# Kernel optimization log

Hardware: AMD Instinct MI355X
Metric: run time of the kernel (lower is better)

The kernel has to match this reference:

```python
import jax, jax.numpy as jnp
import numpy as np

B, C, H, W = 8, 512, 32, 32


def setup_inputs() -> dict:
    key = jax.random.key(0)
    kx, kq, kk, k6 = jax.random.split(key, 4)
    std = 0.02
    return {
        "x": jax.random.normal(kx, (B, C, H, W), dtype=jnp.float32),
        "Wq": jax.random.normal(kq, (C, C), dtype=jnp.float32) * std,
        "bq": jnp.zeros((C,), dtype=jnp.float32),
        "Wk": jax.random.normal(kk, (C, C), dtype=jnp.float32) * std,
        "bk": jnp.zeros((C,), dtype=jnp.float32),
        "W6": jax.random.normal(k6, (C, C), dtype=jnp.float32) * std,
        "b6": jnp.zeros((C,), dtype=jnp.float32),
    }


def reference(x, Wq, bq, Wk, bk, W6, b6):
    b, c, h, w = x.shape
    hw = h * w
    scale = 1.0 / (c ** 0.5)
    # [B, HW, C] token-major view of the feature map
    xf = jnp.transpose(x.reshape(b, c, hw), (0, 2, 1))
    # 1x1 convs are per-pixel linear layers (weight layout: [C_out, C_in])
    q = xf @ Wq.T + bq                      # [B, HW, C]
    k = xf @ Wk.T + bk                      # [B, HW, C]
    # cross-batch attention scores: every pixel attends to every pixel of every image
    scores = q.reshape(b * hw, c) @ k.reshape(b * hw, c).T   # [B*HW, B*HW]
    s = scores.reshape(b * hw, b, hw)
    # per-query: max response within each image, then mean over images
    xw = jnp.max(s, axis=-1).mean(axis=-1)  # [B*HW]
    xw = xw.reshape(b, hw) * scale
    xw = jax.nn.softmax(xw, axis=-1).reshape(b, 1, h, w)
    x5 = x * xw                             # spatial gating
    # final 1x1 conv
    of = jnp.transpose(x5.reshape(b, c, hw), (0, 2, 1)) @ W6.T + b6
    return jnp.transpose(of, (0, 2, 1)).reshape(b, c, h, w)
```

## Files before the change

### kernel.cpp

```cpp
#include <hip/hip_runtime.h>


typedef __attribute__((ext_vector_type(8))) short bf16x8;
typedef __attribute__((ext_vector_type(4))) float f32x4;
typedef __attribute__((ext_vector_type(2))) long long i64x2;

__device__ __forceinline__ unsigned short f2bf(float f) {
  unsigned u = __builtin_bit_cast(unsigned, f);
  u += 0x7FFFu + ((u >> 16) & 1u);
  return (unsigned short)(u >> 16);
}

__device__ __forceinline__ unsigned char f2e4m3(float x) {
  unsigned u = __builtin_bit_cast(unsigned, x);
  unsigned char s = (unsigned char)((u >> 24) & 0x80u);
  unsigned a = u & 0x7FFFFFFFu;
  if (a >= 0x43E00000u) return s | 0x7Eu;
  if (a < 0x3C800000u) {
    float q = __builtin_bit_cast(float, a) * 512.f;
    int m = (int)(q + 0.5f);
    return s | (unsigned char)m;
  }
  unsigned r = a + 0x7FFFFu + ((a >> 20) & 1u);
  int e = (int)((r >> 23) & 0xFF) - 127;
  if (e > 8) return s | 0x7Eu;
  unsigned m3 = (r >> 20) & 0x7u;
  return s | (unsigned char)(((e + 7) << 3) | m3);
}

__device__ __forceinline__ void gload_lds16(const void* g, void* l) {
  __builtin_amdgcn_global_load_lds(
      (const __attribute__((address_space(1))) unsigned int*)g,
      (__attribute__((address_space(3))) unsigned int*)l, 16, 0, 0);
}

__global__ __launch_bounds__(256) void prep(const float* __restrict__ x,
                                            const float* __restrict__ Wq,
                                            const float* __restrict__ Wk,
                                            const float* __restrict__ W6,
                                            short* __restrict__ xt,
                                            short* __restrict__ wcat) {
  const int bid = blockIdx.x, u = threadIdx.x;
  if (bid < 1024) {
    const int p0 = (bid & 15) * 64, c0 = ((bid >> 4) & 7) * 64, b = bid >> 7;
    __shared__ float t[64][65];
    {
      const int p4 = u & 15, cr = u >> 4;
      for (int cc = 0; cc < 4; ++cc) {
        const int c = cc * 16 + cr;
        const float4 v = *(const float4*)&x[((size_t)(b * 512 + c0 + c)) * 1024 + p0 + p4 * 4];
        t[p4 * 4 + 0][c] = v.x; t[p4 * 4 + 1][c] = v.y;
        t[p4 * 4 + 2][c] = v.z; t[p4 * 4 + 3][c] = v.w;
      }
    }
    __syncthreads();
    {
      const int c4 = u & 15, pr = u >> 4;
      for (int pp = 0; pp < 4; ++pp) {
        const int p = pp * 16 + pr;
        ushort4 o;
        o.x = f2bf(t[p][c4 * 4 + 0]); o.y = f2bf(t[p][c4 * 4 + 1]);
        o.z = f2bf(t[p][c4 * 4 + 2]); o.w = f2bf(t[p][c4 * 4 + 3]);
        *(ushort4*)&xt[((size_t)(b * 1024 + p0 + p)) * 512 + c0 + c4 * 4] = o;
      }
    }
  } else {
    const int i = (bid - 1024) * 256 + u;
    const int idx = i * 4;
    const float* src = (idx < 262144) ? Wq : (idx < 524288) ? Wk : W6;
    const float4 v = *(const float4*)&src[idx & 262143];
    ushort4 o;
    o.x = f2bf(v.x); o.y = f2bf(v.y); o.z = f2bf(v.z); o.w = f2bf(v.w);
    *(ushort4*)&wcat[idx] = o;
  }
}

__global__ __launch_bounds__(256) void gemm_qk(const short* __restrict__ xt,
                                               const short* __restrict__ wcat,
                                               const float* __restrict__ bq,
                                               const float* __restrict__ bk,
                                               unsigned char* __restrict__ qk8) {
  __shared__ short lds_a[128 * 64];
  __shared__ short lds_b[128 * 64];
  const int tid = threadIdx.x, w = tid >> 6, lane = tid & 63;
  const int wr = w >> 1, wc = w & 1;
  const int quad = lane >> 4, lcol = lane & 15;
  const int srow = lane & 15, skq = lane >> 4;
  const int m0 = blockIdx.x * 128, n0 = blockIdx.y * 128;

  f32x4 acc[4][4];
#pragma unroll
  for (int i = 0; i < 4; ++i)
#pragma unroll
    for (int j = 0; j < 4; ++j)
#pragma unroll
      for (int r = 0; r < 4; ++r) acc[i][j][r] = 0.f;

  const short* Abase = xt + (size_t)(m0 + srow) * 512 + skq * 8;
  const short* Bbase = wcat + (size_t)(n0 + srow) * 512 + skq * 8;

  for (int kt = 0; kt < 8; ++kt) {
    const int kb = kt * 64;
    __syncthreads();
#pragma unroll
    for (int gg = 0; gg < 2; ++gg) {
      const int g = w + gg * 4;
      gload_lds16(Abase + (size_t)(g * 16) * 512 + kb,      lds_a + g * 1024);
      gload_lds16(Abase + (size_t)(g * 16) * 512 + kb + 32, lds_a + g * 1024 + 512);
      gload_lds16(Bbase + (size_t)(g * 16) * 512 + kb,      lds_b + g * 1024);
      gload_lds16(Bbase + (size_t)(g * 16) * 512 + kb + 32, lds_b + g * 1024 + 512);
    }
    __syncthreads();
#pragma unroll
    for (int h = 0; h < 2; ++h) {
      bf16x8 af[4], bf[4];
#pragma unroll
      for (int i = 0; i < 4; ++i)
        af[i] = *(const bf16x8*)&lds_a[(wr * 4 + i) * 1024 + h * 512 + lane * 8];
#pragma unroll
      for (int j = 0; j < 4; ++j)
        bf[j] = *(const bf16x8*)&lds_b[(wc * 4 + j) * 1024 + h * 512 + lane * 8];
#pragma unroll
      for (int i = 0; i < 4; ++i)
#pragma unroll
        for (int j = 0; j < 4; ++j)
          acc[i][j] = __builtin_amdgcn_mfma_f32_16x16x32_bf16(af[i], bf[j], acc[i][j], 0, 0, 0);
    }
  }

  const float* bias = (blockIdx.y >= 4) ? bk : bq;
#pragma unroll
  for (int i = 0; i < 4; ++i)
#pragma unroll
    for (int j = 0; j < 4; ++j) {
      const int row = m0 + wr * 64 + i * 16 + quad * 4;
      const int col = n0 + wc * 64 + j * 16 + lcol;
      const float bv = bias[col & 511];
#pragma unroll
      for (int r = 0; r < 4; ++r)
        qk8[(size_t)(row + r) * 1024 + col] = f2e4m3(acc[i][j][r] + bv);
    }
}

__global__ __launch_bounds__(256) void gemm_scores(const unsigned char* __restrict__ qk8,
                                                   float* __restrict__ wsmx) {
  __shared__ unsigned char lds_b[32768];
  const int tid = threadIdx.x, w = tid >> 6, lane = tid & 63;
  const int quad = lane >> 4, lcol = lane & 15;
  const int srow = lane & 15, skb = (lane >> 4) * 16;
  const int m0 = blockIdx.x * 128, n0 = blockIdx.y * 128;

  f32x4 acc[2][8];
#pragma unroll
  for (int rg = 0; rg < 2; ++rg)
#pragma unroll
    for (int j = 0; j < 8; ++j)
#pragma unroll
      for (int r = 0; r < 4; ++r) acc[rg][j][r] = 0.f;

  const unsigned char* Abase = qk8 + (size_t)(m0 + w * 32 + srow) * 1024 + skb;
  const unsigned char* Bbase = qk8 + (size_t)(n0 + srow) * 1024 + 512 + skb;

#pragma unroll
  for (int kh = 0; kh < 2; ++kh) {
    __syncthreads();
#pragma unroll
    for (int jj = 0; jj < 2; ++jj) {
      const int j = w * 2 + jj;
#pragma unroll
      for (int kb = 0; kb < 4; ++kb)
        gload_lds16(Bbase + (size_t)(j * 16) * 1024 + kh * 256 + kb * 64,
                    lds_b + j * 4096 + kb * 1024);
    }
    i64x2 af[2][4];
#pragma unroll
    for (int rg = 0; rg < 2; ++rg)
#pragma unroll
      for (int kb = 0; kb < 4; ++kb)
        af[rg][kb] = *(const i64x2*)(Abase + (size_t)rg * 16384 + kh * 256 + kb * 64);
    __syncthreads();
#pragma unroll
    for (int kb = 0; kb < 4; ++kb) {
#pragma unroll
      for (int j = 0; j < 8; ++j) {
        const i64x2 bf = *(const i64x2*)&lds_b[j * 4096 + kb * 1024 + lane * 16];
#pragma unroll
        for (int rg = 0; rg < 2; ++rg) {
          acc[rg][j] = __builtin_amdgcn_mfma_f32_16x16x32_fp8_fp8(
              af[rg][kb].x, bf.x, acc[rg][j], 0, 0, 0);
          acc[rg][j] = __builtin_amdgcn_mfma_f32_16x16x32_fp8_fp8(
              af[rg][kb].y, bf.y, acc[rg][j], 0, 0, 0);
        }
      }
    }
  }

#pragma unroll
  for (int rg = 0; rg < 2; ++rg) {
#pragma unroll
    for (int r = 0; r < 4; ++r) {
      float v = acc[rg][0][r];
#pragma unroll
      for (int j = 1; j < 8; ++j) v = fmaxf(v, acc[rg][j][r]);
#pragma unroll
      for (int off = 1; off < 16; off <<= 1) v = fmaxf(v, __shfl_xor(v, off));
      if (lcol == 0)
        wsmx[(size_t)blockIdx.y * 8192 + m0 + w * 32 + rg * 16 + quad * 4 + r] = v;
    }
  }
}

__global__ __launch_bounds__(1024) void softmax_xw(const float* __restrict__ wsmx,
                                                   float* __restrict__ xw) {
  const int b = blockIdx.x, p = threadIdx.x;
  const int m = b * 1024 + p;
  float s = 0.f;
#pragma unroll
  for (int img = 0; img < 8; ++img) {
    float mx = -1e30f;
#pragma unroll
    for (int t = 0; t < 8; ++t) mx = fmaxf(mx, wsmx[(size_t)(img * 8 + t) * 8192 + m]);
    s += mx;
  }
  const float logit = s * 0.005524271728019903f;
  __shared__ float red[16];
  float v = logit;
#pragma unroll
  for (int off = 32; off >= 1; off >>= 1) v = fmaxf(v, __shfl_xor(v, off));
  if ((p & 63) == 0) red[p >> 6] = v;
  __syncthreads();
  float bmax = red[0];
#pragma unroll
  for (int t = 1; t < 16; ++t) bmax = fmaxf(bmax, red[t]);
  const float e = expf(logit - bmax);
  float sv = e;
#pragma unroll
  for (int off = 32; off >= 1; off >>= 1) sv += __shfl_xor(sv, off);
  __syncthreads();
  if ((p & 63) == 0) red[p >> 6] = sv;
  __syncthreads();
  float bsum = 0.f;
#pragma unroll
  for (int t = 0; t < 16; ++t) bsum += red[t];
  xw[m] = e / bsum;
}

__global__ __launch_bounds__(256) void gemm_out(const short* __restrict__ xt,
                                                const short* __restrict__ wcat,
                                                const float* __restrict__ xw,
                                                const float* __restrict__ b6,
                                                float* __restrict__ out) {
  __shared__ short lds_a[64 * 64];
  __shared__ short lds_b[64 * 64];
  const int tid = threadIdx.x, w = tid >> 6, lane = tid & 63;
  const int wr = w >> 1, wc = w & 1;
  const int quad = lane >> 4, lcol = lane & 15;
  const int srow = lane & 15, skq = lane >> 4;
  const int m0 = blockIdx.x * 64, n0 = blockIdx.y * 64;

  f32x4 acc[2][2];
#pragma unroll
  for (int i = 0; i < 2; ++i)
#pragma unroll
    for (int j = 0; j < 2; ++j)
#pragma unroll
      for (int r = 0; r < 4; ++r) acc[i][j][r] = 0.f;

  const short* Abase = xt + (size_t)(m0 + w * 16 + srow) * 512 + skq * 8;
  const short* Bbase = wcat + (size_t)(1024 + n0 + w * 16 + srow) * 512 + skq * 8;

  for (int kt = 0; kt < 8; ++kt) {
    const int kb = kt * 64;
    __syncthreads();
    gload_lds16(Abase + kb,      lds_a + w * 1024);
    gload_lds16(Abase + kb + 32, lds_a + w * 1024 + 512);
    gload_lds16(Bbase + kb,      lds_b + w * 1024);
    gload_lds16(Bbase + kb + 32, lds_b + w * 1024 + 512);
    __syncthreads();
#pragma unroll
    for (int h = 0; h < 2; ++h) {
      bf16x8 af[2], bf[2];
#pragma unroll
      for (int i = 0; i < 2; ++i)
        af[i] = *(const bf16x8*)&lds_a[(wr * 2 + i) * 1024 + h * 512 + lane * 8];
#pragma unroll
      for (int j = 0; j < 2; ++j)
        bf[j] = *(const bf16x8*)&lds_b[(wc * 2 + j) * 1024 + h * 512 + lane * 8];
#pragma unroll
      for (int i = 0; i < 2; ++i)
#pragma unroll
        for (int j = 0; j < 2; ++j)
          acc[i][j] = __builtin_amdgcn_mfma_f32_16x16x32_bf16(af[i], bf[j], acc[i][j], 0, 0, 0);
    }
  }

#pragma unroll
  for (int i = 0; i < 2; ++i) {
    const int mbase = m0 + wr * 32 + i * 16 + quad * 4;
    const int b = mbase >> 10, p = mbase & 1023;
    const float4 wv = *(const float4*)&xw[mbase];
#pragma unroll
    for (int j = 0; j < 2; ++j) {
      const int col = n0 + wc * 32 + j * 16 + lcol;
      const float bias = b6[col];
      float4 o;
      o.x = acc[i][j][0] * wv.x + bias;
      o.y = acc[i][j][1] * wv.y + bias;
      o.z = acc[i][j][2] * wv.z + bias;
      o.w = acc[i][j][3] * wv.w + bias;
      *(float4*)&out[((size_t)(b * 512 + col)) * 1024 + p] = o;
    }
  }
}

extern "C" void kernel_launch(void* const* d_in, const int* in_sizes, int n_in,
                              void* d_out, int out_size, void* d_ws, size_t ws_size,
                              hipStream_t stream) {
  const float* x  = (const float*)d_in[0];
  const float* Wq = (const float*)d_in[1];
  const float* bq = (const float*)d_in[2];
  const float* Wk = (const float*)d_in[3];
  const float* bk = (const float*)d_in[4];
  const float* W6 = (const float*)d_in[5];
  const float* b6 = (const float*)d_in[6];
  float* out = (float*)d_out;

  char* ws = (char*)d_ws;
  short* xt          = (short*)(ws + 0);
  short* wcat        = (short*)(ws + 8388608);
  unsigned char* qk8 = (unsigned char*)(ws + 10485760);
  float* wsmx        = (float*)(ws + 18874368);
  float* xw          = (float*)(ws + 20971520);

  prep<<<1792, 256, 0, stream>>>(x, Wq, Wk, W6, xt, wcat);
  gemm_qk<<<dim3(64, 8), 256, 0, stream>>>(xt, wcat, bq, bk, qk8);
  gemm_scores<<<dim3(64, 64), 256, 0, stream>>>(qk8, wsmx);
  softmax_xw<<<8, 1024, 0, stream>>>(wsmx, xw);
  gemm_out<<<dim3(128, 8), 256, 0, stream>>>(xt, wcat, xw, b6, out);
}
```

Measured before the change: 191.6 us.

## Fold output projection into QK GEMM and use scaled fp8 MFMA for scores

The W6 projection is now computed in the first GEMM launch as extra column tiles, written as fp32 z. The output becomes a transpose-and-scale epilogue, valid because per-pixel gating commutes with the 1x1 conv. The scores GEMM switches from 16x16x32 fp8 MFMA to the 16x16x128 f8f6f4 scaled MFMA with unit scales, which halves the LDS staging buffer and issues fewer, larger instructions. This removes a separate bf16 GEMM launch but adds a 16 MB fp32 z write and reread.

```diff
diff --git a/kernel.cpp b/kernel.cpp
--- a/kernel.cpp
+++ b/kernel.cpp
@@ -3,7 +3,8 @@
 
 typedef __attribute__((ext_vector_type(8))) short bf16x8;
 typedef __attribute__((ext_vector_type(4))) float f32x4;
-typedef __attribute__((ext_vector_type(2))) long long i64x2;
+typedef __attribute__((ext_vector_type(4))) int i32x4;
+typedef __attribute__((ext_vector_type(8))) int i32x8;
 
 __device__ __forceinline__ unsigned short f2bf(float f) {
   unsigned u = __builtin_bit_cast(unsigned, f);
@@ -75,11 +76,12 @@
   }
 }
 
-__global__ __launch_bounds__(256) void gemm_qk(const short* __restrict__ xt,
-                                               const short* __restrict__ wcat,
-                                               const float* __restrict__ bq,
-                                               const float* __restrict__ bk,
-                                               unsigned char* __restrict__ qk8) {
+__global__ __launch_bounds__(256) void gemm_qkz(const short* __restrict__ xt,
+                                                const short* __restrict__ wcat,
+                                                const float* __restrict__ bq,
+                                                const float* __restrict__ bk,
+                                                unsigned char* __restrict__ qk8,
+                                                float* __restrict__ z) {
   __shared__ short lds_a[128 * 64];
   __shared__ short lds_b[128 * 64];
   const int tid = threadIdx.x, w = tid >> 6, lane = tid & 63;
@@ -128,23 +130,37 @@
     }
   }
 
-  const float* bias = (blockIdx.y >= 4) ? bk : bq;
-#pragma unroll
-  for (int i = 0; i < 4; ++i)
-#pragma unroll
-    for (int j = 0; j < 4; ++j) {
-      const int row = m0 + wr * 64 + i * 16 + quad * 4;
-      const int col = n0 + wc * 64 + j * 16 + lcol;
-      const float bv = bias[col & 511];
-#pragma unroll
-      for (int r = 0; r < 4; ++r)
-        qk8[(size_t)(row + r) * 1024 + col] = f2e4m3(acc[i][j][r] + bv);
-    }
+  const int region = (int)blockIdx.y >> 2;
+  if (region < 2) {
+    const float* bias = region ? bk : bq;
+#pragma unroll
+    for (int i = 0; i < 4; ++i)
+#pragma unroll
+      for (int j = 0; j < 4; ++j) {
+        const int row = m0 + wr * 64 + i * 16 + quad * 4;
+        const int col = n0 + wc * 64 + j * 16 + lcol;
+        const float bv = bias[col & 511];
+#pragma unroll
+        for (int r = 0; r < 4; ++r)
+          qk8[(size_t)(row + r) * 1024 + col] = f2e4m3(acc[i][j][r] + bv);
+      }
+  } else {
+#pragma unroll
+    for (int i = 0; i < 4; ++i)
+#pragma unroll
+      for (int j = 0; j < 4; ++j) {
+        const int row = m0 + wr * 64 + i * 16 + quad * 4;
+        const int col = n0 - 1024 + wc * 64 + j * 16 + lcol;
+#pragma unroll
+        for (int r = 0; r < 4; ++r)
+          z[(size_t)(row + r) * 512 + col] = acc[i][j][r];
+      }
+  }
 }
 
 __global__ __launch_bounds__(256) void gemm_scores(const unsigned char* __restrict__ qk8,
                                                    float* __restrict__ wsmx) {
-  __shared__ unsigned char lds_b[32768];
+  __shared__ unsigned char lds_b[16384];
   const int tid = threadIdx.x, w = tid >> 6, lane = tid & 63;
   const int quad = lane >> 4, lcol = lane & 15;
   const int srow = lane & 15, skb = (lane >> 4) * 16;
@@ -162,36 +178,34 @@
   const unsigned char* Bbase = qk8 + (size_t)(n0 + srow) * 1024 + 512 + skb;
 
 #pragma unroll
-  for (int kh = 0; kh < 2; ++kh) {
+  for (int kh = 0; kh < 4; ++kh) {
+    const int kb = kh * 128;
     __syncthreads();
 #pragma unroll
     for (int jj = 0; jj < 2; ++jj) {
       const int j = w * 2 + jj;
 #pragma unroll
-      for (int kb = 0; kb < 4; ++kb)
-        gload_lds16(Bbase + (size_t)(j * 16) * 1024 + kh * 256 + kb * 64,
-                    lds_b + j * 4096 + kb * 1024);
-    }
-    i64x2 af[2][4];
-#pragma unroll
-    for (int rg = 0; rg < 2; ++rg)
-#pragma unroll
-      for (int kb = 0; kb < 4; ++kb)
-        af[rg][kb] = *(const i64x2*)(Abase + (size_t)rg * 16384 + kh * 256 + kb * 64);
-    __syncthreads();
-#pragma unroll
-    for (int kb = 0; kb < 4; ++kb) {
-#pragma unroll
-      for (int j = 0; j < 8; ++j) {
-        const i64x2 bf = *(const i64x2*)&lds_b[j * 4096 + kb * 1024 + lane * 16];
-#pragma unroll
-        for (int rg = 0; rg < 2; ++rg) {
-          acc[rg][j] = __builtin_amdgcn_mfma_f32_16x16x32_fp8_fp8(
-              af[rg][kb].x, bf.x, acc[rg][j], 0, 0, 0);
-          acc[rg][j] = __builtin_amdgcn_mfma_f32_16x16x32_fp8_fp8(
-              af[rg][kb].y, bf.y, acc[rg][j], 0, 0, 0);
-        }
-      }
+      for (int h = 0; h < 2; ++h)
+        gload_lds16(Bbase + (size_t)(j * 16) * 1024 + kb + h * 64,
+                    lds_b + j * 2048 + h * 1024);
+    }
+    i32x8 af[2];
+#pragma unroll
+    for (int rg = 0; rg < 2; ++rg) {
+      const i32x4 lo = *(const i32x4*)(Abase + (size_t)rg * 16384 + kb);
+      const i32x4 hi = *(const i32x4*)(Abase + (size_t)rg * 16384 + kb + 64);
+      af[rg] = __builtin_shufflevector(lo, hi, 0, 1, 2, 3, 4, 5, 6, 7);
+    }
+    __syncthreads();
+#pragma unroll
+    for (int j = 0; j < 8; ++j) {
+      const i32x4 blo = *(const i32x4*)&lds_b[j * 2048 + lane * 16];
+      const i32x4 bhi = *(const i32x4*)&lds_b[j * 2048 + 1024 + lane * 16];
+      const i32x8 bf = __builtin_shufflevector(blo, bhi, 0, 1, 2, 3, 4, 5, 6, 7);
+#pragma unroll
+      for (int rg = 0; rg < 2; ++rg)
+        acc[rg][j] = __builtin_amdgcn_mfma_scale_f32_16x16x128_f8f6f4(
+            af[rg], bf, acc[rg][j], 0, 0, 0, 127, 0, 127);
     }
   }
 
@@ -245,70 +259,37 @@
   xw[m] = e / bsum;
 }
 
-__global__ __launch_bounds__(256) void gemm_out(const short* __restrict__ xt,
-                                                const short* __restrict__ wcat,
-                                                const float* __restrict__ xw,
-                                                const float* __restrict__ b6,
-                                                float* __restrict__ out) {
-  __shared__ short lds_a[64 * 64];
-  __shared__ short lds_b[64 * 64];
-  const int tid = threadIdx.x, w = tid >> 6, lane = tid & 63;
-  const int wr = w >> 1, wc = w & 1;
-  const int quad = lane >> 4, lcol = lane & 15;
-  const int srow = lane & 15, skq = lane >> 4;
-  const int m0 = blockIdx.x * 64, n0 = blockIdx.y * 64;
-
-  f32x4 acc[2][2];
-#pragma unroll
-  for (int i = 0; i < 2; ++i)
-#pragma unroll
-    for (int j = 0; j < 2; ++j)
-#pragma unroll
-      for (int r = 0; r < 4; ++r) acc[i][j][r] = 0.f;
-
-  const short* Abase = xt + (size_t)(m0 + w * 16 + srow) * 512 + skq * 8;
-  const short* Bbase = wcat + (size_t)(1024 + n0 + w * 16 + srow) * 512 + skq * 8;
-
-  for (int kt = 0; kt < 8; ++kt) {
-    const int kb = kt * 64;
-    __syncthreads();
-    gload_lds16(Abase + kb,      lds_a + w * 1024);
-    gload_lds16(Abase + kb + 32, lds_a + w * 1024 + 512);
-    gload_lds16(Bbase + kb,      lds_b + w * 1024);
-    gload_lds16(Bbase + kb + 32, lds_b + w * 1024 + 512);
-    __syncthreads();
-#pragma unroll
-    for (int h = 0; h < 2; ++h) {
-      bf16x8 af[2], bf[2];
-#pragma unroll
-      for (int i = 0; i < 2; ++i)
-        af[i] = *(const bf16x8*)&lds_a[(wr * 2 + i) * 1024 + h * 512 + lane * 8];
-#pragma unroll
-      for (int j = 0; j < 2; ++j)
-        bf[j] = *(const bf16x8*)&lds_b[(wc * 2 + j) * 1024 + h * 512 + lane * 8];
-#pragma unroll
-      for (int i = 0; i < 2; ++i)
-#pragma unroll
-        for (int j = 0; j < 2; ++j)
-          acc[i][j] = __builtin_amdgcn_mfma_f32_16x16x32_bf16(af[i], bf[j], acc[i][j], 0, 0, 0);
-    }
-  }
-
-#pragma unroll
-  for (int i = 0; i < 2; ++i) {
-    const int mbase = m0 + wr * 32 + i * 16 + quad * 4;
-    const int b = mbase >> 10, p = mbase & 1023;
-    const float4 wv = *(const float4*)&xw[mbase];
-#pragma unroll
-    for (int j = 0; j < 2; ++j) {
-      const int col = n0 + wc * 32 + j * 16 + lcol;
-      const float bias = b6[col];
+__global__ __launch_bounds__(256) void epilogue_out(const float* __restrict__ z,
+                                                    const float* __restrict__ xw,
+                                                    const float* __restrict__ b6,
+                                                    float* __restrict__ out) {
+  const int p0 = blockIdx.x * 64, c0 = blockIdx.y * 64, b = blockIdx.z;
+  __shared__ float t[64][65];
+  const int u = threadIdx.x;
+  {
+    const int c4 = u & 15, pr = u >> 4;
+    for (int pp = 0; pp < 4; ++pp) {
+      const int p = pp * 16 + pr;
+      const float4 v = *(const float4*)&z[((size_t)(b * 1024 + p0 + p)) * 512 + c0 + c4 * 4];
+      t[c4 * 4 + 0][p] = v.x;
+      t[c4 * 4 + 1][p] = v.y;
+      t[c4 * 4 + 2][p] = v.z;
+      t[c4 * 4 + 3][p] = v.w;
+    }
+  }
+  __syncthreads();
+  {
+    const int p4 = u & 15, cr = u >> 4;
+    const float4 wv = *(const float4*)&xw[b * 1024 + p0 + p4 * 4];
+    for (int cc = 0; cc < 4; ++cc) {
+      const int co = cc * 16 + cr;
+      const float bias = b6[c0 + co];
       float4 o;
-      o.x = acc[i][j][0] * wv.x + bias;
-      o.y = acc[i][j][1] * wv.y + bias;
-      o.z = acc[i][j][2] * wv.z + bias;
-      o.w = acc[i][j][3] * wv.w + bias;
-      *(float4*)&out[((size_t)(b * 512 + col)) * 1024 + p] = o;
+      o.x = t[co][p4 * 4 + 0] * wv.x + bias;
+      o.y = t[co][p4 * 4 + 1] * wv.y + bias;
+      o.z = t[co][p4 * 4 + 2] * wv.z + bias;
+      o.w = t[co][p4 * 4 + 3] * wv.w + bias;
+      *(float4*)&out[((size_t)(b * 512 + c0 + co)) * 1024 + p0 + p4 * 4] = o;
     }
   }
 }
@@ -329,12 +310,13 @@
   short* xt          = (short*)(ws + 0);
   short* wcat        = (short*)(ws + 8388608);
   unsigned char* qk8 = (unsigned char*)(ws + 10485760);
-  float* wsmx        = (float*)(ws + 18874368);
-  float* xw          = (float*)(ws + 20971520);
+  float* z           = (float*)(ws + 18874368);
+  float* wsmx        = (float*)(ws + 35651584);
+  float* xw          = (float*)(ws + 37748736);
 
   prep<<<1792, 256, 0, stream>>>(x, Wq, Wk, W6, xt, wcat);
-  gemm_qk<<<dim3(64, 8), 256, 0, stream>>>(xt, wcat, bq, bk, qk8);
+  gemm_qkz<<<dim3(64, 12), 256, 0, stream>>>(xt, wcat, bq, bk, qk8, z);
   gemm_scores<<<dim3(64, 64), 256, 0, stream>>>(qk8, wsmx);
   softmax_xw<<<8, 1024, 0, stream>>>(wsmx, xw);
-  gemm_out<<<dim3(128, 8), 256, 0, stream>>>(xt, wcat, xw, b6, out);
-}
+  epilogue_out<<<dim3(16, 8, 8), 256, 0, stream>>>(z, xw, b6, out);
+}
```

Result: slower. 250.2 us (+30.6%).

## Drop LDS staging in all GEMMs and load MFMA operands directly from global

Applied to the files above, without the earlier changes.

Removes shared-memory tiles and global_load_lds staging from gemm_qk, gemm_scores and gemm_out. Each wave now loads its MFMA operands straight from global memory into registers, with no __syncthreads between tiles. gemm_qk is also retiled from 128x128 to 64x128 blocks, doubling its grid, and each wave owns a 16-row strip. This removes barrier and LDS round-trip overhead, but it relies on L1/L2 for reuse of B across waves and may issue more redundant global traffic.

```diff
diff --git a/kernel.cpp b/kernel.cpp
--- a/kernel.cpp
+++ b/kernel.cpp
@@ -26,12 +26,6 @@
   if (e > 8) return s | 0x7Eu;
   unsigned m3 = (r >> 20) & 0x7u;
   return s | (unsigned char)(((e + 7) << 3) | m3);
-}
-
-__device__ __forceinline__ void gload_lds16(const void* g, void* l) {
-  __builtin_amdgcn_global_load_lds(
-      (const __attribute__((address_space(1))) unsigned int*)g,
-      (__attribute__((address_space(3))) unsigned int*)l, 16, 0, 0);
 }
 
 __global__ __launch_bounds__(256) void prep(const float* __restrict__ x,
@@ -80,74 +74,46 @@
                                                const float* __restrict__ bq,
                                                const float* __restrict__ bk,
                                                unsigned char* __restrict__ qk8) {
-  __shared__ short lds_a[128 * 64];
-  __shared__ short lds_b[128 * 64];
   const int tid = threadIdx.x, w = tid >> 6, lane = tid & 63;
-  const int wr = w >> 1, wc = w & 1;
   const int quad = lane >> 4, lcol = lane & 15;
-  const int srow = lane & 15, skq = lane >> 4;
-  const int m0 = blockIdx.x * 128, n0 = blockIdx.y * 128;
-
-  f32x4 acc[4][4];
-#pragma unroll
-  for (int i = 0; i < 4; ++i)
-#pragma unroll
-    for (int j = 0; j < 4; ++j)
-#pragma unroll
-      for (int r = 0; r < 4; ++r) acc[i][j][r] = 0.f;
-
-  const short* Abase = xt + (size_t)(m0 + srow) * 512 + skq * 8;
-  const short* Bbase = wcat + (size_t)(n0 + srow) * 512 + skq * 8;
-
-  for (int kt = 0; kt < 8; ++kt) {
-    const int kb = kt * 64;
-    __syncthreads();
-#pragma unroll
-    for (int gg = 0; gg < 2; ++gg) {
-      const int g = w + gg * 4;
-      gload_lds16(Abase + (size_t)(g * 16) * 512 + kb,      lds_a + g * 1024);
-      gload_lds16(Abase + (size_t)(g * 16) * 512 + kb + 32, lds_a + g * 1024 + 512);
-      gload_lds16(Bbase + (size_t)(g * 16) * 512 + kb,      lds_b + g * 1024);
-      gload_lds16(Bbase + (size_t)(g * 16) * 512 + kb + 32, lds_b + g * 1024 + 512);
-    }
-    __syncthreads();
-#pragma unroll
-    for (int h = 0; h < 2; ++h) {
-      bf16x8 af[4], bf[4];
-#pragma unroll
-      for (int i = 0; i < 4; ++i)
-        af[i] = *(const bf16x8*)&lds_a[(wr * 4 + i) * 1024 + h * 512 + lane * 8];
-#pragma unroll
-      for (int j = 0; j < 4; ++j)
-        bf[j] = *(const bf16x8*)&lds_b[(wc * 4 + j) * 1024 + h * 512 + lane * 8];
-#pragma unroll
-      for (int i = 0; i < 4; ++i)
-#pragma unroll
-        for (int j = 0; j < 4; ++j)
-          acc[i][j] = __builtin_amdgcn_mfma_f32_16x16x32_bf16(af[i], bf[j], acc[i][j], 0, 0, 0);
+  const int m0 = blockIdx.x * 64, n0 = blockIdx.y * 128;
+
+  f32x4 acc[8];
+#pragma unroll
+  for (int j = 0; j < 8; ++j)
+#pragma unroll
+    for (int r = 0; r < 4; ++r) acc[j][r] = 0.f;
+
+  const short* Abase = xt + (size_t)(m0 + w * 16 + lcol) * 512 + quad * 8;
+  const short* Bbase = wcat + (size_t)(n0 + lcol) * 512 + quad * 8;
+
+#pragma unroll
+  for (int kt = 0; kt < 16; ++kt) {
+    const int kb = kt * 32;
+    const bf16x8 af = *(const bf16x8*)(Abase + kb);
+#pragma unroll
+    for (int j = 0; j < 8; ++j) {
+      const bf16x8 bf = *(const bf16x8*)(Bbase + (size_t)(j * 16) * 512 + kb);
+      acc[j] = __builtin_amdgcn_mfma_f32_16x16x32_bf16(af, bf, acc[j], 0, 0, 0);
     }
   }
 
   const float* bias = (blockIdx.y >= 4) ? bk : bq;
-#pragma unroll
-  for (int i = 0; i < 4; ++i)
-#pragma unroll
-    for (int j = 0; j < 4; ++j) {
-      const int row = m0 + wr * 64 + i * 16 + quad * 4;
-      const int col = n0 + wc * 64 + j * 16 + lcol;
-      const float bv = bias[col & 511];
-#pragma unroll
-      for (int r = 0; r < 4; ++r)
-        qk8[(size_t)(row + r) * 1024 + col] = f2e4m3(acc[i][j][r] + bv);
-    }
+  const int row = m0 + w * 16 + quad * 4;
+#pragma unroll
+  for (int j = 0; j < 8; ++j) {
+    const int col = n0 + j * 16 + lcol;
+    const float bv = bias[col & 511];
+#pragma unroll
+    for (int r = 0; r < 4; ++r)
+      qk8[(size_t)(row + r) * 1024 + col] = f2e4m3(acc[j][r] + bv);
+  }
 }
 
 __global__ __launch_bounds__(256) void gemm_scores(const unsigned char* __restrict__ qk8,
                                                    float* __restrict__ wsmx) {
-  __shared__ unsigned char lds_b[32768];
   const int tid = threadIdx.x, w = tid >> 6, lane = tid & 63;
   const int quad = lane >> 4, lcol = lane & 15;
-  const int srow = lane & 15, skb = (lane >> 4) * 16;
   const int m0 = blockIdx.x * 128, n0 = blockIdx.y * 128;
 
   f32x4 acc[2][8];
@@ -158,39 +124,25 @@
 #pragma unroll
       for (int r = 0; r < 4; ++r) acc[rg][j][r] = 0.f;
 
-  const unsigned char* Abase = qk8 + (size_t)(m0 + w * 32 + srow) * 1024 + skb;
-  const unsigned char* Bbase = qk8 + (size_t)(n0 + srow) * 1024 + 512 + skb;
-
-#pragma unroll
-  for (int kh = 0; kh < 2; ++kh) {
-    __syncthreads();
-#pragma unroll
-    for (int jj = 0; jj < 2; ++jj) {
-      const int j = w * 2 + jj;
-#pragma unroll
-      for (int kb = 0; kb < 4; ++kb)
-        gload_lds16(Bbase + (size_t)(j * 16) * 1024 + kh * 256 + kb * 64,
-                    lds_b + j * 4096 + kb * 1024);
-    }
-    i64x2 af[2][4];
+  const unsigned char* Abase = qk8 + (size_t)(m0 + w * 32 + lcol) * 1024 + quad * 16;
+  const unsigned char* Bbase = qk8 + (size_t)(n0 + lcol) * 1024 + 512 + quad * 16;
+
+#pragma unroll
+  for (int c = 0; c < 8; ++c) {
+    const int kb = c * 64;
+    i64x2 af[2];
 #pragma unroll
     for (int rg = 0; rg < 2; ++rg)
-#pragma unroll
-      for (int kb = 0; kb < 4; ++kb)
-        af[rg][kb] = *(const i64x2*)(Abase + (size_t)rg * 16384 + kh * 256 + kb * 64);
-    __syncthreads();
-#pragma unroll
-    for (int kb = 0; kb < 4; ++kb) {
-#pragma unroll
-      for (int j = 0; j < 8; ++j) {
-        const i64x2 bf = *(const i64x2*)&lds_b[j * 4096 + kb * 1024 + lane * 16];
-#pragma unroll
-        for (int rg = 0; rg < 2; ++rg) {
-          acc[rg][j] = __builtin_amdgcn_mfma_f32_16x16x32_fp8_fp8(
-              af[rg][kb].x, bf.x, acc[rg][j], 0, 0, 0);
-          acc[rg][j] = __builtin_amdgcn_mfma_f32_16x16x32_fp8_fp8(
-              af[rg][kb].y, bf.y, acc[rg][j], 0, 0, 0);
-        }
+      af[rg] = *(const i64x2*)(Abase + (size_t)rg * 16384 + kb);
+#pragma unroll
+    for (int j = 0; j < 8; ++j) {
+      const i64x2 bf = *(const i64x2*)(Bbase + (size_t)(j * 16) * 1024 + kb);
+#pragma unroll
+      for (int rg = 0; rg < 2; ++rg) {
+        acc[rg][j] = __builtin_amdgcn_mfma_f32_16x16x32_fp8_fp8(
+            af[rg].x, bf.x, acc[rg][j], 0, 0, 0);
+        acc[rg][j] = __builtin_amdgcn_mfma_f32_16x16x32_fp8_fp8(
+            af[rg].y, bf.y, acc[rg][j], 0, 0, 0);
       }
     }
   }
@@ -250,66 +202,43 @@
                                                 const float* __restrict__ xw,
                                                 const float* __restrict__ b6,
                                                 float* __restrict__ out) {
-  __shared__ short lds_a[64 * 64];
-  __shared__ short lds_b[64 * 64];
   const int tid = threadIdx.x, w = tid >> 6, lane = tid & 63;
-  const int wr = w >> 1, wc = w & 1;
   const int quad = lane >> 4, lcol = lane & 15;
-  const int srow = lane & 15, skq = lane >> 4;
   const int m0 = blockIdx.x * 64, n0 = blockIdx.y * 64;
 
-  f32x4 acc[2][2];
-#pragma unroll
-  for (int i = 0; i < 2; ++i)
-#pragma unroll
-    for (int j = 0; j < 2; ++j)
-#pragma unroll
-      for (int r = 0; r < 4; ++r) acc[i][j][r] = 0.f;
-
-  const short* Abase = xt + (size_t)(m0 + w * 16 + srow) * 512 + skq * 8;
-  const short* Bbase = wcat + (size_t)(1024 + n0 + w * 16 + srow) * 512 + skq * 8;
-
-  for (int kt = 0; kt < 8; ++kt) {
-    const int kb = kt * 64;
-    __syncthreads();
-    gload_lds16(Abase + kb,      lds_a + w * 1024);
-    gload_lds16(Abase + kb + 32, lds_a + w * 1024 + 512);
-    gload_lds16(Bbase + kb,      lds_b + w * 1024);
-    gload_lds16(Bbase + kb + 32, lds_b + w * 1024 + 512);
-    __syncthreads();
-#pragma unroll
-    for (int h = 0; h < 2; ++h) {
-      bf16x8 af[2], bf[2];
-#pragma unroll
-      for (int i = 0; i < 2; ++i)
-        af[i] = *(const bf16x8*)&lds_a[(wr * 2 + i) * 1024 + h * 512 + lane * 8];
-#pragma unroll
-      for (int j = 0; j < 2; ++j)
-        bf[j] = *(const bf16x8*)&lds_b[(wc * 2 + j) * 1024 + h * 512 + lane * 8];
-#pragma unroll
-      for (int i = 0; i < 2; ++i)
-#pragma unroll
-        for (int j = 0; j < 2; ++j)
-          acc[i][j] = __builtin_amdgcn_mfma_f32_16x16x32_bf16(af[i], bf[j], acc[i][j], 0, 0, 0);
-    }
-  }
-
-#pragma unroll
-  for (int i = 0; i < 2; ++i) {
-    const int mbase = m0 + wr * 32 + i * 16 + quad * 4;
-    const int b = mbase >> 10, p = mbase & 1023;
-    const float4 wv = *(const float4*)&xw[mbase];
-#pragma unroll
-    for (int j = 0; j < 2; ++j) {
-      const int col = n0 + wc * 32 + j * 16 + lcol;
-      const float bias = b6[col];
-      float4 o;
-      o.x = acc[i][j][0] * wv.x + bias;
-      o.y = acc[i][j][1] * wv.y + bias;
-      o.z = acc[i][j][2] * wv.z + bias;
-      o.w = acc[i][j][3] * wv.w + bias;
-      *(float4*)&out[((size_t)(b * 512 + col)) * 1024 + p] = o;
-    }
+  f32x4 acc[4];
+#pragma unroll
+  for (int j = 0; j < 4; ++j)
+#pragma unroll
+    for (int r = 0; r < 4; ++r) acc[j][r] = 0.f;
+
+  const short* Abase = xt + (size_t)(m0 + w * 16 + lcol) * 512 + quad * 8;
+  const short* Bbase = wcat + (size_t)(1024 + n0 + lcol) * 512 + quad * 8;
+
+#pragma unroll
+  for (int kt = 0; kt < 16; ++kt) {
+    const int kb = kt * 32;
+    const bf16x8 af = *(const bf16x8*)(Abase + kb);
+#pragma unroll
+    for (int j = 0; j < 4; ++j) {
+      const bf16x8 bf = *(const bf16x8*)(Bbase + (size_t)(j * 16) * 512 + kb);
+      acc[j] = __builtin_amdgcn_mfma_f32_16x16x32_bf16(af, bf, acc[j], 0, 0, 0);
+    }
+  }
+
+  const int mbase = m0 + w * 16 + quad * 4;
+  const int b = mbase >> 10, p = mbase & 1023;
+  const float4 wv = *(const float4*)&xw[mbase];
+#pragma unroll
+  for (int j = 0; j < 4; ++j) {
+    const int col = n0 + j * 16 + lcol;
+    const float bias = b6[col];
+    float4 o;
+    o.x = acc[j][0] * wv.x + bias;
+    o.y = acc[j][1] * wv.y + bias;
+    o.z = acc[j][2] * wv.z + bias;
+    o.w = acc[j][3] * wv.w + bias;
+    *(float4*)&out[((size_t)(b * 512 + col)) * 1024 + p] = o;
   }
 }
 
@@ -333,7 +262,7 @@
   float* xw          = (float*)(ws + 20971520);
 
   prep<<<1792, 256, 0, stream>>>(x, Wq, Wk, W6, xt, wcat);
-  gemm_qk<<<dim3(64, 8), 256, 0, stream>>>(xt, wcat, bq, bk, qk8);
+  gemm_qk<<<dim3(128, 8), 256, 0, stream>>>(xt, wcat, bq, bk, qk8);
   gemm_scores<<<dim3(64, 64), 256, 0, stream>>>(qk8, wsmx);
   softmax_xw<<<8, 1024, 0, stream>>>(wsmx, xw);
   gemm_out<<<dim3(128, 8), 256, 0, stream>>>(xt, wcat, xw, b6, out);
```

Measured after the change: 337.5 us. 76.1% more time.
